# Kernel tuning notes

Measured on AMD Instinct MI355X. Metric: run time of the kernel, lower is better.

The kernel has to match this reference:

```python
import jax, jax.numpy as jnp
import numpy as np

B, T, H, V, N_AT, KC, MAX_NB = 512, 64, 512, 780, 40, 4, 8
NMSG = B * T + 1  # message table size; slot 0 = zero padding vector


def setup_inputs() -> dict:
    key = jax.random.key(0)
    ks = jax.random.split(key, 24)
    s = 0.02
    f32 = jnp.float32
    w = lambda k, shp: jax.random.normal(k, shp, f32) * s
    inp = {}
    inp["node_rep"] = jax.random.normal(ks[0], (B, N_AT, H), f32)
    inp["clique_idx"] = jax.random.randint(ks[1], (B, T, KC), 0, N_AT)
    inp["root_clique_idx"] = jax.random.randint(ks[2], (B, KC), 0, N_AT)
    inp["nei_h_idx"] = jax.random.randint(ks[3], (B, T, MAX_NB), 0, NMSG)
    inp["nei_o_idx"] = jax.random.randint(ks[4], (B, T, MAX_NB), 0, NMSG)
    inp["root_nei_idx"] = jax.random.randint(ks[5], (B, MAX_NB), 0, NMSG)
    inp["direction"] = jax.random.randint(ks[6], (B, T), 0, 2)
    inp["pred_target"] = jax.random.randint(ks[7], (B, T), 0, V)
    inp["W_z_w"] = w(ks[8], (2 * H, H)); inp["W_z_b"] = jnp.zeros((H,), f32)
    inp["W_r_w"] = w(ks[9], (H, H));     inp["W_r_b"] = jnp.zeros((H,), f32)
    inp["U_r_w"] = w(ks[10], (H, H))  # no bias in torch U_r
    inp["W_h_w"] = w(ks[11], (2 * H, H)); inp["W_h_b"] = jnp.zeros((H,), f32)
    inp["W_w"] = w(ks[12], (H, H));     inp["W_b"] = jnp.zeros((H,), f32)
    inp["U_w"] = w(ks[13], (2 * H, H)); inp["U_b"] = jnp.zeros((H,), f32)
    inp["W_o_w"] = w(ks[14], (H, V));   inp["W_o_b"] = jnp.zeros((V,), f32)
    inp["U_s_w"] = w(ks[15], (H, 1));   inp["U_s_b"] = jnp.zeros((1,), f32)
    return inp


def _gru(x, h_nei, W_z_w, W_z_b, W_r_w, W_r_b, U_r_w, W_h_w, W_h_b):
    # x: [B,H]; h_nei: [B,MAX_NB,H]  (tree-GRU from the torch GRU() helper)
    sum_h = h_nei.sum(axis=1)
    z = jax.nn.sigmoid(jnp.concatenate([x, sum_h], axis=1) @ W_z_w + W_z_b)
    r = jax.nn.sigmoid((x @ W_r_w + W_r_b)[:, None, :] + h_nei @ U_r_w)
    sum_g = (r * h_nei).sum(axis=1)
    pre_h = jnp.tanh(jnp.concatenate([x, sum_g], axis=1) @ W_h_w + W_h_b)
    return (1.0 - z) * sum_h + z * pre_h


def reference(node_rep, clique_idx, root_clique_idx, nei_h_idx, nei_o_idx,
              root_nei_idx, direction, pred_target,
              W_z_w, W_z_b, W_r_w, W_r_b, U_r_w, W_h_w, W_h_b,
              W_w, W_b, U_w, U_b, W_o_w, W_o_b, U_s_w, U_s_b):
    dt = node_rep.dtype
    b_ar = jnp.arange(B)
    # x features: sum of node_rep over clique atom indices (torch index_select+sum)
    x_all = node_rep[b_ar[:, None, None], clique_idx].sum(axis=2)      # [B,T,H]
    root_x = node_rep[b_ar[:, None], root_clique_idx].sum(axis=1)      # [B,H]
    msg_ids = b_ar[:, None] * T + jnp.arange(T)[None, :] + 1           # [B,T]
    table0 = jnp.zeros((NMSG, H), dt)                                  # h dict -> flat table

    def step(table, xs):
        x_t, h_idx, o_idx, mid = xs
        h_nei = table[h_idx]                      # [B,MAX_NB,H] gather (excl. parent, pre-padded)
        new_h = _gru(x_t, h_nei, W_z_w, W_z_b, W_r_w, W_r_b, U_r_w, W_h_w, W_h_b)
        o = table[o_idx].sum(axis=1)              # [B,H] all-neighbor sum for stop head
        table = table.at[mid].set(new_h)          # scatter message back (h[x,y] = new_h)
        return table, (new_h, o)

    xs = (x_all.transpose(1, 0, 2), nei_h_idx.transpose(1, 0, 2),
          nei_o_idx.transpose(1, 0, 2), msg_ids.T)
    table, (new_h_all, o_all) = jax.lax.scan(step, table0, xs)
    new_h_all = new_h_all.transpose(1, 0, 2).reshape(B * T, H)         # [BT,H]
    o_all = o_all.transpose(1, 0, 2)                                   # [B,T,H]

    # stop head: all steps + final root step (target 0)
    stop_h = jnp.concatenate([x_all, o_all], axis=2).reshape(B * T, 2 * H)
    root_o = table[root_nei_idx].sum(axis=1)
    root_stop = jnp.concatenate([root_x, root_o], axis=1)
    stop_hiddens = jnp.concatenate([stop_h, root_stop], axis=0)        # [BT+B,2H]
    stop_targets = jnp.concatenate([direction.reshape(-1).astype(dt), jnp.zeros((B,), dt)])
    stop_scores = (jax.nn.relu(stop_hiddens @ U_w + U_b) @ U_s_w + U_s_b)[:, 0]
    # BCEWithLogits, sum reduction, / len(mol_batch)
    stop_loss = jnp.sum(jax.nn.softplus(stop_scores) - stop_scores * stop_targets) / B
    stop_acc = jnp.mean(((stop_scores >= 0).astype(dt) == stop_targets).astype(dt))

    # pred head on new_h where direction == 1
    pred_scores = jax.nn.relu(new_h_all @ W_w + W_b) @ W_o_w + W_o_b   # [BT,V]
    logp = jax.nn.log_softmax(pred_scores, axis=-1)
    tgt = pred_target.reshape(-1)
    ce = -jnp.take_along_axis(logp, tgt[:, None], axis=1)[:, 0]
    pmask = (direction.reshape(-1) == 1).astype(dt)
    pred_loss = jnp.sum(ce * pmask) / B                                # CE sum / len(mol_batch)
    preds = jnp.argmax(pred_scores, axis=1)
    pred_acc = jnp.sum((preds == tgt).astype(dt) * pmask) / jnp.sum(pmask)
    return (pred_loss, stop_loss, pred_acc, stop_acc)
```

## Files before the change

### kernel.cpp

```cpp
#include <hip/hip_runtime.h>
#include <math.h>

constexpr int B    = 512;
constexpr int T    = 64;
constexpr int H    = 512;
constexpr int V    = 780;
constexpr int N_AT = 40;
constexpr int KC   = 4;
constexpr int NB   = 8;
constexpr int BT   = B * T;
constexpr int NMSG = BT + 1;

template<int ASRC, int NSEG, int EPI>
__device__ __forceinline__ void gemm_core(
    float* smem, int bx, int by,
    const float* __restrict__ A1, const float* __restrict__ A2, int lda,
    const float* __restrict__ W, const float* __restrict__ bias,
    float* __restrict__ C, int ldc,
    const int* __restrict__ gidx, int gt, const float* __restrict__ table,
    const float* __restrict__ node_rep, const int* __restrict__ cliq,
    const float* __restrict__ o_all,
    const int* __restrict__ rci, const int* __restrict__ rni,
    const float* __restrict__ Ez, const float* __restrict__ Esh,
    const float* __restrict__ Usw, float* __restrict__ partial)
{
    float* As = smem;
    float* Ws = smem + 32 * 68;
    const int tid  = threadIdx.x;
    const int row0 = bx * 64;
    const int col0 = by * 64;
    const int tm   = tid >> 4;
    const int tn   = tid & 15;

    float acc[4][4] = {};

    const int ar0 = tid >> 5;
    const int ac  = tid & 31;
    const int wk0 = tid >> 6;
    const int wc  = tid & 63;

    for (int seg = 0; seg < NSEG; ++seg) {
        const float* Aseg = seg ? A2 : A1;
        const float* Wseg = W + (size_t)seg * H * H;
        for (int k0 = 0; k0 < H; k0 += 32) {
#pragma unroll
            for (int it = 0; it < 8; ++it) {
                const int r    = ar0 + it * 8;
                const int grow = row0 + r;
                float v;
                if (ASRC == 0) {
                    v = Aseg[(size_t)grow * lda + k0 + ac];
                } else if (ASRC == 1) {
                    const int gi = gidx[((grow >> 3) * T + gt) * NB + (grow & 7)];
                    v = table[(size_t)gi * H + k0 + ac];
                } else if (ASRC == 2) {
                    const int* ci = cliq + (size_t)grow * KC;
                    const int  b  = grow >> 6;
                    v = 0.f;
#pragma unroll
                    for (int j = 0; j < KC; ++j)
                        v += node_rep[((size_t)b * N_AT + ci[j]) * H + k0 + ac];
                } else {
                    if (grow < BT) {
                        if (seg == 0) {
                            const int* ci = cliq + (size_t)grow * KC;
                            const int  b  = grow >> 6;
                            v = 0.f;
#pragma unroll
                            for (int j = 0; j < KC; ++j)
                                v += node_rep[((size_t)b * N_AT + ci[j]) * H + k0 + ac];
                        } else {
                            v = o_all[(size_t)grow * H + k0 + ac];
                        }
                    } else {
                        const int b = grow - BT;
                        v = 0.f;
                        if (seg == 0) {
#pragma unroll
                            for (int j = 0; j < KC; ++j)
                                v += node_rep[((size_t)b * N_AT + rci[b * KC + j]) * H + k0 + ac];
                        } else {
#pragma unroll
                            for (int n = 0; n < NB; ++n)
                                v += table[(size_t)rni[b * NB + n] * H + k0 + ac];
                        }
                    }
                }
                As[(size_t)ac * 68 + r] = v;
                const int kk = wk0 + it * 4;
                Ws[(size_t)kk * 68 + wc] = Wseg[(size_t)(k0 + kk) * H + col0 + wc];
            }
            __syncthreads();
#pragma unroll
            for (int kk = 0; kk < 32; ++kk) {
                float a[4], w[4];
                *(float4*)a = *(const float4*)&As[kk * 68 + tm * 4];
                *(float4*)w = *(const float4*)&Ws[kk * 68 + tn * 4];
#pragma unroll
                for (int i = 0; i < 4; ++i)
#pragma unroll
                    for (int j = 0; j < 4; ++j)
                        acc[i][j] = fmaf(a[i], w[j], acc[i][j]);
            }
            __syncthreads();
        }
    }

    if (EPI == 4) {
        float* sred = smem + 2 * 32 * 68;
#pragma unroll
        for (int i = 0; i < 4; ++i) {
            float s = 0.f;
#pragma unroll
            for (int j = 0; j < 4; ++j) {
                const int ccol = col0 + tn * 4 + j;
                float val = acc[i][j] + bias[ccol];
                val = fmaxf(val, 0.f);
                s += val * Usw[ccol];
            }
            sred[(size_t)(tm * 4 + i) * 17 + tn] = s;
        }
        __syncthreads();
        if (tid < 64) {
            float s = 0.f;
#pragma unroll
            for (int t2 = 0; t2 < 16; ++t2) s += sred[(size_t)tid * 17 + t2];
            partial[(size_t)(row0 + tid) * 8 + by] = s;
        }
    } else {
#pragma unroll
        for (int i = 0; i < 4; ++i) {
            const int r = row0 + tm * 4 + i;
            float out[4];
#pragma unroll
            for (int j = 0; j < 4; ++j) {
                const int ccol = col0 + tn * 4 + j;
                float val = acc[i][j] + (bias ? bias[ccol] : 0.f);
                if (EPI == 1) {
                    val = 1.f / (1.f + expf(-val));
                } else if (EPI == 2) {
                    const float ph = tanhf(val);
                    const float zz = Ez[(size_t)r * H + ccol];
                    const float sh = Esh[(size_t)r * H + ccol];
                    val = (1.f - zz) * sh + zz * ph;
                } else if (EPI == 3) {
                    val = fmaxf(val, 0.f);
                }
                out[j] = val;
            }
            *(float4*)&C[(size_t)r * ldc + col0 + tn * 4] = *(float4*)out;
        }
    }
}

constexpr size_t SM_GEMM = (size_t)(2 * 32 * 68) * 4;
constexpr size_t SM_STOP = (size_t)(2 * 32 * 68 + 64 * 17) * 4;

template<int ASRC, int NSEG, int EPI>
__global__ __launch_bounds__(256)
void gemm_g(const float* __restrict__ A1, const float* __restrict__ A2, int lda,
            const float* __restrict__ W, const float* __restrict__ bias,
            float* __restrict__ C, int ldc,
            const int* __restrict__ gidx, int gt, const float* __restrict__ table,
            const float* __restrict__ node_rep, const int* __restrict__ cliq,
            const float* __restrict__ o_all,
            const int* __restrict__ rci, const int* __restrict__ rni,
            const float* __restrict__ Ez, const float* __restrict__ Esh,
            const float* __restrict__ Usw, float* __restrict__ partial)
{
    extern __shared__ float smem[];
    gemm_core<ASRC, NSEG, EPI>(smem, blockIdx.x, blockIdx.y, A1, A2, lda, W, bias,
                               C, ldc, gidx, gt, table, node_rep, cliq, o_all,
                               rci, rni, Ez, Esh, Usw, partial);
}

__global__ __launch_bounds__(256)
void step1_kernel(const int* __restrict__ nei_h, int t, const float* __restrict__ table,
                  const float* __restrict__ Urw, float* __restrict__ hU,
                  const float* __restrict__ xs, const float* __restrict__ Wzw,
                  const float* __restrict__ Wzb, float* __restrict__ zb)
{
    extern __shared__ float smem[];
    if (blockIdx.x < 64) {
        gemm_core<1, 1, 0>(smem, blockIdx.x, blockIdx.y, nullptr, nullptr, 0,
                           Urw, nullptr, hU, H, nei_h, t, table,
                           nullptr, nullptr, nullptr, nullptr, nullptr,
                           nullptr, nullptr, nullptr, nullptr);
    } else {
        gemm_core<0, 2, 1>(smem, blockIdx.x - 64, blockIdx.y, xs, xs + H, 2 * H,
                           Wzw, Wzb, zb, H, nullptr, 0, nullptr,
                           nullptr, nullptr, nullptr, nullptr, nullptr,
                           nullptr, nullptr, nullptr, nullptr);
    }
}

__global__ __launch_bounds__(256)
void pre2_kernel(const float* __restrict__ node_rep, const int* __restrict__ clique_idx,
                 const int* __restrict__ nei_h, const int* __restrict__ nei_o,
                 const float* __restrict__ table,
                 float* __restrict__ xs, float* __restrict__ hs, float* __restrict__ ss,
                 float* __restrict__ sumh, float* __restrict__ oDst, int oStride, int t)
{
    const int i = blockIdx.x * 256 + threadIdx.x;
    const int b = i >> 9, h = i & 511;
    const int* ci = clique_idx + ((size_t)b * T + t) * KC;
    float x = 0.f;
#pragma unroll
    for (int k = 0; k < KC; ++k)
        x += node_rep[((size_t)b * N_AT + ci[k]) * H + h];
    const int* hi = nei_h + ((size_t)b * T + t) * NB;
    const int* oi = nei_o + ((size_t)b * T + t) * NB;
    float sh = 0.f, so = 0.f;
#pragma unroll
    for (int n = 0; n < NB; ++n) {
        sh += table[(size_t)hi[n] * H + h];
        so += table[(size_t)oi[n] * H + h];
    }
    xs[(size_t)b * 1024 + h]       = x;
    xs[(size_t)b * 1024 + 512 + h] = sh;
    hs[(size_t)b * 1024 + h]       = x;
    ss[(size_t)b * 1024 + h]       = x;
    sumh[i] = sh;
    oDst[(size_t)b * oStride + h] = so;
}

__global__ __launch_bounds__(256)
void rsum2_kernel(const float* __restrict__ xrP, int xrStride,
                  const float* __restrict__ hU, const float* __restrict__ table,
                  const int* __restrict__ nei_h, float* __restrict__ hs, int t)
{
    const int i = blockIdx.x * 256 + threadIdx.x;
    const int b = i >> 9, h = i & 511;
    const int* hi = nei_h + ((size_t)b * T + t) * NB;
    const float xrv = xrP[(size_t)b * xrStride + h];
    float s = 0.f;
#pragma unroll
    for (int n = 0; n < NB; ++n) {
        const float hu = hU[((size_t)b * NB + n) * H + h];
        const float r  = 1.f / (1.f + expf(-(xrv + hu)));
        s += r * table[(size_t)hi[n] * H + h];
    }
    hs[(size_t)b * 1024 + 512 + h] = s;
}

__global__ __launch_bounds__(256)
void rootpre_kernel(const float* __restrict__ node_rep, const int* __restrict__ rci,
                    const int* __restrict__ rni, const float* __restrict__ table,
                    float* __restrict__ ss)
{
    const int i = blockIdx.x * 256 + threadIdx.x;
    const int b = i >> 9, h = i & 511;
    float x = 0.f;
#pragma unroll
    for (int k = 0; k < KC; ++k)
        x += node_rep[((size_t)b * N_AT + rci[b * KC + k]) * H + h];
    float so = 0.f;
#pragma unroll
    for (int n = 0; n < NB; ++n)
        so += table[(size_t)rni[b * NB + n] * H + h];
    ss[(size_t)b * 1024 + h]       = x;
    ss[(size_t)b * 1024 + 512 + h] = so;
}

__global__ __launch_bounds__(64)
void stopdot_kernel(const float* __restrict__ s1, const float* __restrict__ Usw,
                    const float* __restrict__ Usb,
                    float* __restrict__ out, int outStride, int outBase)
{
    const int b = blockIdx.x;
    const int lane = threadIdx.x;
    const float* row = s1 + (size_t)b * H;
    float s = 0.f;
    for (int h = lane; h < H; h += 64) s += row[h] * Usw[h];
#pragma unroll
    for (int off = 32; off; off >>= 1) s += __shfl_down(s, off);
    if (lane == 0) out[outBase + b * outStride] = s + Usb[0];
}

__global__ __launch_bounds__(256)
void stoploss_kernel(const float* __restrict__ scores, const int* __restrict__ direction,
                     float* __restrict__ accum)
{
    const int i = blockIdx.x * 256 + threadIdx.x;
    float loss = 0.f, acc = 0.f;
    if (i < BT + B) {
        const float s   = scores[i];
        const float tgt = (i < BT) ? (float)direction[i] : 0.f;
        loss = fmaxf(s, 0.f) - s * tgt + log1pf(expf(-fabsf(s)));
        const float p = (s >= 0.f) ? 1.f : 0.f;
        acc = (p == tgt) ? 1.f : 0.f;
    }
#pragma unroll
    for (int off = 32; off; off >>= 1) {
        loss += __shfl_down(loss, off);
        acc  += __shfl_down(acc, off);
    }
    if ((threadIdx.x & 63) == 0) {
        atomicAdd(&accum[3], loss);
        atomicAdd(&accum[4], acc);
    }
}

__global__ __launch_bounds__(256)
void stopfin_kernel(const float* __restrict__ partial, const float* __restrict__ Usb,
                    const int* __restrict__ direction, float* __restrict__ accum)
{
    const int i = blockIdx.x * 256 + threadIdx.x;
    float loss = 0.f, acc = 0.f;
    {
        float s = Usb[0];
#pragma unroll
        for (int cb = 0; cb < 8; ++cb) s += partial[(size_t)i * 8 + cb];
        const float tgt = (i < BT) ? (float)direction[i] : 0.f;
        loss = fmaxf(s, 0.f) - s * tgt + log1pf(expf(-fabsf(s)));
        const float p = (s >= 0.f) ? 1.f : 0.f;
        acc = (p == tgt) ? 1.f : 0.f;
    }
#pragma unroll
    for (int off = 32; off; off >>= 1) {
        loss += __shfl_down(loss, off);
        acc  += __shfl_down(acc, off);
    }
    if ((threadIdx.x & 63) == 0) {
        atomicAdd(&accum[3], loss);
        atomicAdd(&accum[4], acc);
    }
}

__global__ __launch_bounds__(256)
void ce_kernel(const float* __restrict__ s1_all, const float* __restrict__ Wo,
               const float* __restrict__ Wob, const int* __restrict__ direction,
               const int* __restrict__ ptgt, float* __restrict__ accum)
{
    __shared__ float s1T[512 * 34];
    __shared__ float Ws[32 * 68];
    __shared__ float blk[3];
    const int tid  = threadIdx.x;
    const int row0 = blockIdx.x * 32;

    for (int idx = tid; idx < 32 * 512; idx += 256) {
        const int r = idx >> 9, k = idx & 511;
        s1T[(size_t)k * 34 + r] = s1_all[(size_t)(row0 + r) * H + k];
    }
    if (tid < 3) blk[tid] = 0.f;
    __syncthreads();

    const int tm = tid >> 4, tn = tid & 15;
    const int tgt0 = ptgt[row0 + tm * 2];
    const int tgt1 = ptgt[row0 + tm * 2 + 1];
    float m0 = -1e30f, m1 = -1e30f, ss0 = 0.f, ss1 = 0.f, st0 = 0.f, st1 = 0.f;
    float bv0 = -1e30f, bv1 = -1e30f;
    int   bj0 = 0, bj1 = 0;

    for (int ct = 0; ct < 13; ++ct) {
        const int col0 = ct * 64;
        float acc[2][4] = {};
        for (int k0 = 0; k0 < 512; k0 += 32) {
#pragma unroll
            for (int it = 0; it < 8; ++it) {
                const int idx = tid + it * 256;
                const int kk = idx >> 6, cc = idx & 63;
                const int col = col0 + cc;
                Ws[(size_t)kk * 68 + cc] = (col < V) ? Wo[(size_t)(k0 + kk) * V + col] : 0.f;
            }
            __syncthreads();
#pragma unroll
            for (int kk = 0; kk < 32; ++kk) {
                const float a0 = s1T[(size_t)(k0 + kk) * 34 + tm * 2];
                const float a1 = s1T[(size_t)(k0 + kk) * 34 + tm * 2 + 1];
                float w[4];
                *(float4*)w = *(const float4*)&Ws[kk * 68 + tn * 4];
#pragma unroll
                for (int j = 0; j < 4; ++j) {
                    acc[0][j] = fmaf(a0, w[j], acc[0][j]);
                    acc[1][j] = fmaf(a1, w[j], acc[1][j]);
                }
            }
            __syncthreads();
        }
#pragma unroll
        for (int j = 0; j < 4; ++j) {
            const int col = col0 + tn * 4 + j;
            if (col < V) {
                const float wb  = Wob[col];
                const float sc0 = acc[0][j] + wb;
                const float sc1 = acc[1][j] + wb;
                if (sc0 > m0) { ss0 = ss0 * expf(m0 - sc0) + 1.f; m0 = sc0; }
                else          { ss0 += expf(sc0 - m0); }
                if (sc1 > m1) { ss1 = ss1 * expf(m1 - sc1) + 1.f; m1 = sc1; }
                else          { ss1 += expf(sc1 - m1); }
                if (sc0 > bv0) { bv0 = sc0; bj0 = col; }
                if (sc1 > bv1) { bv1 = sc1; bj1 = col; }
                if (col == tgt0) st0 = sc0;
                if (col == tgt1) st1 = sc1;
            }
        }
    }

#pragma unroll
    for (int off = 1; off < 16; off <<= 1) {
        float om, os;
        om = __shfl_xor(m0, off); os = __shfl_xor(ss0, off);
        { const float nm = fmaxf(m0, om); ss0 = ss0 * expf(m0 - nm) + os * expf(om - nm); m0 = nm; }
        om = __shfl_xor(m1, off); os = __shfl_xor(ss1, off);
        { const float nm = fmaxf(m1, om); ss1 = ss1 * expf(m1 - nm) + os * expf(om - nm); m1 = nm; }
        float obv; int obj;
        obv = __shfl_xor(bv0, off); obj = __shfl_xor(bj0, off);
        if (obv > bv0 || (obv == bv0 && obj < bj0)) { bv0 = obv; bj0 = obj; }
        obv = __shfl_xor(bv1, off); obj = __shfl_xor(bj1, off);
        if (obv > bv1 || (obv == bv1 && obj < bj1)) { bv1 = obv; bj1 = obj; }
        st0 += __shfl_xor(st0, off);
        st1 += __shfl_xor(st1, off);
    }
    if (tn == 0) {
        float ce_s = 0.f, cnt = 0.f, corr = 0.f;
        {
            const int row = row0 + tm * 2;
            if (direction[row] == 1) {
                ce_s += (m0 + logf(ss0)) - st0; cnt += 1.f;
                corr += (bj0 == tgt0) ? 1.f : 0.f;
            }
        }
        {
            const int row = row0 + tm * 2 + 1;
            if (direction[row] == 1) {
                ce_s += (m1 + logf(ss1)) - st1; cnt += 1.f;
                corr += (bj1 == tgt1) ? 1.f : 0.f;
            }
        }
        atomicAdd(&blk[0], ce_s); atomicAdd(&blk[1], cnt); atomicAdd(&blk[2], corr);
    }
    __syncthreads();
    if (tid == 0) {
        atomicAdd(&accum[0], blk[0]);
        atomicAdd(&accum[1], blk[1]);
        atomicAdd(&accum[2], blk[2]);
    }
}

constexpr int PH_ROWS = 8;
__global__ __launch_bounds__(256)
void predhead_kernel(const float* __restrict__ table,
                     const float* __restrict__ Ww, const float* __restrict__ Wb,
                     const float* __restrict__ Wo, const float* __restrict__ Wob,
                     const int* __restrict__ direction, const int* __restrict__ ptgt,
                     float* __restrict__ accum)
{
    __shared__ float hs[PH_ROWS][520];
    __shared__ float s1s[PH_ROWS][520];
    const int row0 = blockIdx.x * PH_ROWS;
    const int tid  = threadIdx.x;
    for (int i = tid; i < PH_ROWS * H; i += 256) {
        const int r = i >> 9, c = i & 511;
        hs[r][c] = table[(size_t)(row0 + r + 1) * H + c];
    }
    __syncthreads();
    const int r  = tid >> 5;
    const int tx = tid & 31;
    for (int j = 0; j < 16; ++j) {
        const int c = tx + j * 32;
        float acc = Wb[c];
        for (int k = 0; k < H; ++k) acc += hs[r][k] * Ww[(size_t)k * H + c];
        s1s[r][c] = fmaxf(acc, 0.f);
    }
    __syncthreads();
    const int row = row0 + r;
    const int tgt = ptgt[row];
    float m = -1e30f, ssum = 0.f, stgt = 0.f;
    float bestv = -1e30f; int bestj = 0;
    for (int v = tx; v < V; v += 32) {
        float sc = Wob[v];
        const float* wcol = Wo + v;
        for (int k = 0; k < H; ++k) sc += s1s[r][k] * wcol[(size_t)k * V];
        if (sc > m) { ssum = ssum * expf(m - sc) + 1.f; m = sc; }
        else        { ssum += expf(sc - m); }
        if (sc > bestv) { bestv = sc; bestj = v; }
        if (v == tgt) stgt = sc;
    }
#pragma unroll
    for (int off = 1; off < 32; off <<= 1) {
        const float om = __shfl_xor(m, off);
        const float os = __shfl_xor(ssum, off);
        const float nm = fmaxf(m, om);
        ssum = ssum * expf(m - nm) + os * expf(om - nm);
        m = nm;
        const float obv = __shfl_xor(bestv, off);
        const int   obj = __shfl_xor(bestj, off);
        if (obv > bestv || (obv == bestv && obj < bestj)) { bestv = obv; bestj = obj; }
        stgt += __shfl_xor(stgt, off);
    }
    if (tx == 0) {
        const float ce   = (m + logf(ssum)) - stgt;
        const float mask = (direction[row] == 1) ? 1.f : 0.f;
        const float corr = (bestj == tgt) ? 1.f : 0.f;
        atomicAdd(&accum[0], ce * mask);
        atomicAdd(&accum[1], mask);
        atomicAdd(&accum[2], corr * mask);
    }
}

__global__ void finalize_kernel(const float* __restrict__ accum, float* __restrict__ out)
{
    if (threadIdx.x == 0) {
        out[0] = accum[0] / (float)B;
        out[1] = accum[3] / (float)B;
        out[2] = accum[2] / accum[1];
        out[3] = accum[4] / (float)(BT + B);
    }
}

extern "C" void kernel_launch(void* const* d_in, const int* in_sizes, int n_in,
                              void* d_out, int out_size, void* d_ws, size_t ws_size,
                              hipStream_t stream)
{
    (void)in_sizes; (void)n_in; (void)out_size;

    const float* node_rep        = (const float*)d_in[0];
    const int*   clique_idx      = (const int*)d_in[1];
    const int*   root_clique_idx = (const int*)d_in[2];
    const int*   nei_h_idx       = (const int*)d_in[3];
    const int*   nei_o_idx       = (const int*)d_in[4];
    const int*   root_nei_idx    = (const int*)d_in[5];
    const int*   direction       = (const int*)d_in[6];
    const int*   pred_target     = (const int*)d_in[7];
    const float* W_z_w = (const float*)d_in[8];
    const float* W_z_b = (const float*)d_in[9];
    const float* W_r_w = (const float*)d_in[10];
    const float* W_r_b = (const float*)d_in[11];
    const float* U_r_w = (const float*)d_in[12];
    const float* W_h_w = (const float*)d_in[13];
    const float* W_h_b = (const float*)d_in[14];
    const float* W_w   = (const float*)d_in[15];
    const float* W_b   = (const float*)d_in[16];
    const float* U_w   = (const float*)d_in[17];
    const float* U_b   = (const float*)d_in[18];
    const float* W_o_w = (const float*)d_in[19];
    const float* W_o_b = (const float*)d_in[20];
    const float* U_s_w = (const float*)d_in[21];
    const float* U_s_b = (const float*)d_in[22];

    float* ws = (float*)d_ws;
    size_t off = 0;
    auto alloc = [&](size_t n) { float* p = ws + off; off += n; return p; };

    float* table  = alloc((size_t)NMSG * H);
    float* hU     = alloc((size_t)B * NB * H);
    float* xs     = alloc((size_t)B * 2 * H);
    float* hs     = alloc((size_t)B * 2 * H);
    float* ss     = alloc((size_t)B * 2 * H);
    float* sumh   = alloc((size_t)B * H);
    float* zb     = alloc((size_t)B * H);
    float* xr     = alloc((size_t)B * H);
    float* stop_scores = alloc(BT + B);
    float* accum  = alloc(8);

    const size_t availF = ws_size / sizeof(float);
    float *s1_all = nullptr, *o_all = nullptr, *partial = nullptr, *xr_all = nullptr;
    if (off + (size_t)BT * H <= availF)                 s1_all = alloc((size_t)BT * H);
    if (off + (size_t)BT * H + (size_t)(BT + B) * 8 <= availF) {
        o_all   = alloc((size_t)BT * H);
        partial = alloc((size_t)(BT + B) * 8);
    }
    if (off + (size_t)BT * H <= availF)                 xr_all = alloc((size_t)BT * H);

    hipMemsetAsync(table, 0, (size_t)NMSG * H * sizeof(float), stream);
    hipMemsetAsync(accum, 0, 8 * sizeof(float), stream);

    const int  BH_blocks = (B * H) / 256;
    const dim3 gSmall(8, 8);
    const dim3 gStep(72, 8);

    if (xr_all) {
        gemm_g<2, 1, 0><<<dim3(BT / 64, 8), 256, SM_GEMM, stream>>>(
            nullptr, nullptr, 0, W_r_w, W_r_b, xr_all, H,
            nullptr, 0, nullptr, node_rep, clique_idx,
            nullptr, nullptr, nullptr, nullptr, nullptr, nullptr, nullptr);
    }

    for (int t = 0; t < T; ++t) {
        float* oDst    = o_all ? (o_all + (size_t)t * H) : (ss + H);
        const int oStr = o_all ? (T * H) : (2 * H);
        pre2_kernel<<<BH_blocks, 256, 0, stream>>>(node_rep, clique_idx, nei_h_idx,
                                                   nei_o_idx, table, xs, hs, ss,
                                                   sumh, oDst, oStr, t);
        step1_kernel<<<gStep, 256, SM_GEMM, stream>>>(nei_h_idx, t, table, U_r_w, hU,
                                                      xs, W_z_w, W_z_b, zb);
        if (!xr_all) {
            gemm_g<0, 1, 0><<<gSmall, 256, SM_GEMM, stream>>>(
                xs, nullptr, 2 * H, W_r_w, W_r_b, xr, H,
                nullptr, 0, nullptr, nullptr, nullptr,
                nullptr, nullptr, nullptr, nullptr, nullptr, nullptr, nullptr);
        }
        const float* xrP   = xr_all ? (xr_all + (size_t)t * H) : xr;
        const int    xrStr = xr_all ? (T * H) : H;
        rsum2_kernel<<<BH_blocks, 256, 0, stream>>>(xrP, xrStr, hU, table,
                                                    nei_h_idx, hs, t);
        gemm_g<0, 2, 2><<<gSmall, 256, SM_GEMM, stream>>>(
            hs, hs + H, 2 * H, W_h_w, W_h_b, table + (size_t)(t + 1) * H, T * H,
            nullptr, 0, nullptr, nullptr, nullptr,
            nullptr, nullptr, nullptr, zb, sumh, nullptr, nullptr);
        if (!o_all) {
            gemm_g<0, 2, 3><<<gSmall, 256, SM_GEMM, stream>>>(
                ss, ss + H, 2 * H, U_w, U_b, zb, H,
                nullptr, 0, nullptr, nullptr, nullptr,
                nullptr, nullptr, nullptr, nullptr, nullptr, nullptr, nullptr);
            stopdot_kernel<<<B, 64, 0, stream>>>(zb, U_s_w, U_s_b, stop_scores, T, t);
        }
    }

    if (o_all) {
        gemm_g<3, 2, 4><<<dim3((BT + B) / 64, 8), 256, SM_STOP, stream>>>(
            nullptr, nullptr, 0, U_w, U_b, nullptr, 0,
            nullptr, 0, table, node_rep, clique_idx,
            o_all, root_clique_idx, root_nei_idx, nullptr, nullptr, U_s_w, partial);
        stopfin_kernel<<<(BT + B) / 256, 256, 0, stream>>>(partial, U_s_b, direction, accum);
    } else {
        rootpre_kernel<<<BH_blocks, 256, 0, stream>>>(node_rep, root_clique_idx,
                                                      root_nei_idx, table, ss);
        gemm_g<0, 2, 3><<<gSmall, 256, SM_GEMM, stream>>>(
            ss, ss + H, 2 * H, U_w, U_b, zb, H,
            nullptr, 0, nullptr, nullptr, nullptr,
            nullptr, nullptr, nullptr, nullptr, nullptr, nullptr, nullptr);
        stopdot_kernel<<<B, 64, 0, stream>>>(zb, U_s_w, U_s_b, stop_scores, 1, BT);
        stoploss_kernel<<<(BT + B + 255) / 256, 256, 0, stream>>>(stop_scores, direction, accum);
    }

    if (s1_all) {
        gemm_g<0, 1, 3><<<dim3(BT / 64, 8), 256, SM_GEMM, stream>>>(
            table + H, nullptr, H, W_w, W_b, s1_all, H,
            nullptr, 0, nullptr, nullptr, nullptr,
            nullptr, nullptr, nullptr, nullptr, nullptr, nullptr, nullptr);
        ce_kernel<<<BT / 32, 256, 0, stream>>>(s1_all, W_o_w, W_o_b,
                                               direction, pred_target, accum);
    } else {
        predhead_kernel<<<BT / PH_ROWS, 256, 0, stream>>>(table, W_w, W_b, W_o_w, W_o_b,
                                                          direction, pred_target, accum);
    }

    finalize_kernel<<<1, 64, 0, stream>>>(accum, (float*)d_out);
}
```

Baseline: 13.48 ms.

## Fuse per-step gather and reset-gate kernels into GEMM A-tile loaders

Removes the separate pre2 and rsum2 elementwise kernels from each time step. Their gathers (clique sums, neighbour message sums, sigmoid-gated reset sums) now run inside the GEMM A-tile loading of a combined stepA kernel and of the W_h GEMM. The W_r GEMM and the nei_o gather become extra block ranges of stepA. This halves launches per step and drops the xs/hs staging buffers. The cost is that gather and expf work is recomputed by every column block of each GEMM, and the h-GEMM runs on only 64 blocks. Neighbour rows belonging to the current step are explicitly zeroed, because those rows are written concurrently by the same kernel.

```diff
diff --git a/kernel.cpp b/kernel.cpp
--- a/kernel.cpp
+++ b/kernel.cpp
@@ -22,7 +22,9 @@
     const float* __restrict__ o_all,
     const int* __restrict__ rci, const int* __restrict__ rni,
     const float* __restrict__ Ez, const float* __restrict__ Esh,
-    const float* __restrict__ Usw, float* __restrict__ partial)
+    const float* __restrict__ Usw, float* __restrict__ partial,
+    const float* __restrict__ xrP, int xrStride,
+    const float* __restrict__ hUin, float* __restrict__ sumhOut)
 {
     float* As = smem;
     float* Ws = smem + 32 * 68;
@@ -60,7 +62,7 @@
 #pragma unroll
                     for (int j = 0; j < KC; ++j)
                         v += node_rep[((size_t)b * N_AT + ci[j]) * H + k0 + ac];
-                } else {
+                } else if (ASRC == 3) {
                     if (grow < BT) {
                         if (seg == 0) {
                             const int* ci = cliq + (size_t)grow * KC;
@@ -83,6 +85,45 @@
 #pragma unroll
                             for (int n = 0; n < NB; ++n)
                                 v += table[(size_t)rni[b * NB + n] * H + k0 + ac];
+                        }
+                    }
+                } else if (ASRC == 5) {
+                    const int b = grow;
+                    if (seg == 0) {
+                        const int* ci = cliq + ((size_t)b * T + gt) * KC;
+                        v = 0.f;
+#pragma unroll
+                        for (int j = 0; j < KC; ++j)
+                            v += node_rep[((size_t)b * N_AT + ci[j]) * H + k0 + ac];
+                    } else {
+                        const int* hi = gidx + ((size_t)b * T + gt) * NB;
+                        v = 0.f;
+#pragma unroll
+                        for (int n = 0; n < NB; ++n)
+                            v += table[(size_t)hi[n] * H + k0 + ac];
+                        if (sumhOut && by == 0)
+                            sumhOut[(size_t)b * H + k0 + ac] = v;
+                    }
+                } else {
+                    const int b = grow;
+                    if (seg == 0) {
+                        const int* ci = cliq + ((size_t)b * T + gt) * KC;
+                        v = 0.f;
+#pragma unroll
+                        for (int j = 0; j < KC; ++j)
+                            v += node_rep[((size_t)b * N_AT + ci[j]) * H + k0 + ac];
+                    } else {
+                        const int* hi = gidx + ((size_t)b * T + gt) * NB;
+                        const float xrv = xrP[(size_t)b * xrStride + k0 + ac];
+                        v = 0.f;
+#pragma unroll
+                        for (int n = 0; n < NB; ++n) {
+                            const int idx = hi[n];
+                            const float hu = hUin[((size_t)b * NB + n) * H + k0 + ac];
+                            const float rr = 1.f / (1.f + expf(-(xrv + hu)));
+                            float hv = table[(size_t)idx * H + k0 + ac];
+                            if (idx != 0 && ((idx - 1) & 63) == gt) hv = 0.f;
+                            v += rr * hv;
                         }
                     }
                 }
@@ -166,81 +207,61 @@
             const float* __restrict__ o_all,
             const int* __restrict__ rci, const int* __restrict__ rni,
             const float* __restrict__ Ez, const float* __restrict__ Esh,
-            const float* __restrict__ Usw, float* __restrict__ partial)
+            const float* __restrict__ Usw, float* __restrict__ partial,
+            const float* __restrict__ xrP, int xrStride,
+            const float* __restrict__ hUin, float* __restrict__ sumhOut)
 {
     extern __shared__ float smem[];
     gemm_core<ASRC, NSEG, EPI>(smem, blockIdx.x, blockIdx.y, A1, A2, lda, W, bias,
                                C, ldc, gidx, gt, table, node_rep, cliq, o_all,
-                               rci, rni, Ez, Esh, Usw, partial);
+                               rci, rni, Ez, Esh, Usw, partial,
+                               xrP, xrStride, hUin, sumhOut);
 }
 
 __global__ __launch_bounds__(256)
-void step1_kernel(const int* __restrict__ nei_h, int t, const float* __restrict__ table,
+void stepA_kernel(const int* __restrict__ nei_h, const int* __restrict__ nei_o, int t,
+                  const float* __restrict__ table, const float* __restrict__ node_rep,
+                  const int* __restrict__ cliq,
                   const float* __restrict__ Urw, float* __restrict__ hU,
-                  const float* __restrict__ xs, const float* __restrict__ Wzw,
-                  const float* __restrict__ Wzb, float* __restrict__ zb)
+                  const float* __restrict__ Wzw, const float* __restrict__ Wzb,
+                  float* __restrict__ zb, float* __restrict__ sumh,
+                  float* __restrict__ xtDst, float* __restrict__ oDst, int xoStride,
+                  const float* __restrict__ Wrw, const float* __restrict__ Wrb,
+                  float* __restrict__ xrOut)
 {
     extern __shared__ float smem[];
-    if (blockIdx.x < 64) {
-        gemm_core<1, 1, 0>(smem, blockIdx.x, blockIdx.y, nullptr, nullptr, 0,
-                           Urw, nullptr, hU, H, nei_h, t, table,
-                           nullptr, nullptr, nullptr, nullptr, nullptr,
-                           nullptr, nullptr, nullptr, nullptr);
+    const int bx = blockIdx.x, by = blockIdx.y;
+    if (bx < 64) {
+        gemm_core<1, 1, 0>(smem, bx, by, nullptr, nullptr, 0, Urw, nullptr, hU, H,
+                           nei_h, t, table, nullptr, nullptr, nullptr, nullptr, nullptr,
+                           nullptr, nullptr, nullptr, nullptr, nullptr, 0, nullptr, nullptr);
+    } else if (bx < 72) {
+        gemm_core<5, 2, 1>(smem, bx - 64, by, nullptr, nullptr, 0, Wzw, Wzb, zb, H,
+                           nei_h, t, table, node_rep, cliq, nullptr, nullptr, nullptr,
+                           nullptr, nullptr, nullptr, nullptr, nullptr, 0, nullptr, sumh);
+    } else if (bx < 200) {
+        const int og = (bx - 72) * 8 + by;
+        const int i  = og * 256 + threadIdx.x;
+        const int b  = i >> 9, h = i & 511;
+        const int* oi = nei_o + ((size_t)b * T + t) * NB;
+        float so = 0.f;
+#pragma unroll
+        for (int n = 0; n < NB; ++n)
+            so += table[(size_t)oi[n] * H + h];
+        oDst[(size_t)b * xoStride + h] = so;
+        if (xtDst) {
+            const int* ci = cliq + ((size_t)b * T + t) * KC;
+            float x = 0.f;
+#pragma unroll
+            for (int j = 0; j < KC; ++j)
+                x += node_rep[((size_t)b * N_AT + ci[j]) * H + h];
+            xtDst[(size_t)b * xoStride + h] = x;
+        }
     } else {
-        gemm_core<0, 2, 1>(smem, blockIdx.x - 64, blockIdx.y, xs, xs + H, 2 * H,
-                           Wzw, Wzb, zb, H, nullptr, 0, nullptr,
-                           nullptr, nullptr, nullptr, nullptr, nullptr,
-                           nullptr, nullptr, nullptr, nullptr);
-    }
-}
-
-__global__ __launch_bounds__(256)
-void pre2_kernel(const float* __restrict__ node_rep, const int* __restrict__ clique_idx,
-                 const int* __restrict__ nei_h, const int* __restrict__ nei_o,
-                 const float* __restrict__ table,
-                 float* __restrict__ xs, float* __restrict__ hs, float* __restrict__ ss,
-                 float* __restrict__ sumh, float* __restrict__ oDst, int oStride, int t)
-{
-    const int i = blockIdx.x * 256 + threadIdx.x;
-    const int b = i >> 9, h = i & 511;
-    const int* ci = clique_idx + ((size_t)b * T + t) * KC;
-    float x = 0.f;
-#pragma unroll
-    for (int k = 0; k < KC; ++k)
-        x += node_rep[((size_t)b * N_AT + ci[k]) * H + h];
-    const int* hi = nei_h + ((size_t)b * T + t) * NB;
-    const int* oi = nei_o + ((size_t)b * T + t) * NB;
-    float sh = 0.f, so = 0.f;
-#pragma unroll
-    for (int n = 0; n < NB; ++n) {
-        sh += table[(size_t)hi[n] * H + h];
-        so += table[(size_t)oi[n] * H + h];
-    }
-    xs[(size_t)b * 1024 + h]       = x;
-    xs[(size_t)b * 1024 + 512 + h] = sh;
-    hs[(size_t)b * 1024 + h]       = x;
-    ss[(size_t)b * 1024 + h]       = x;
-    sumh[i] = sh;
-    oDst[(size_t)b * oStride + h] = so;
-}
-
-__global__ __launch_bounds__(256)
-void rsum2_kernel(const float* __restrict__ xrP, int xrStride,
-                  const float* __restrict__ hU, const float* __restrict__ table,
-                  const int* __restrict__ nei_h, float* __restrict__ hs, int t)
-{
-    const int i = blockIdx.x * 256 + threadIdx.x;
-    const int b = i >> 9, h = i & 511;
-    const int* hi = nei_h + ((size_t)b * T + t) * NB;
-    const float xrv = xrP[(size_t)b * xrStride + h];
-    float s = 0.f;
-#pragma unroll
-    for (int n = 0; n < NB; ++n) {
-        const float hu = hU[((size_t)b * NB + n) * H + h];
-        const float r  = 1.f / (1.f + expf(-(xrv + hu)));
-        s += r * table[(size_t)hi[n] * H + h];
-    }
-    hs[(size_t)b * 1024 + 512 + h] = s;
+        gemm_core<5, 1, 0>(smem, bx - 200, by, nullptr, nullptr, 0, Wrw, Wrb, xrOut, H,
+                           nei_h, t, table, node_rep, cliq, nullptr, nullptr, nullptr,
+                           nullptr, nullptr, nullptr, nullptr, nullptr, 0, nullptr, nullptr);
+    }
 }
 
 __global__ __launch_bounds__(256)
@@ -545,8 +566,6 @@
 
     float* table  = alloc((size_t)NMSG * H);
     float* hU     = alloc((size_t)B * NB * H);
-    float* xs     = alloc((size_t)B * 2 * H);
-    float* hs     = alloc((size_t)B * 2 * H);
     float* ss     = alloc((size_t)B * 2 * H);
     float* sumh   = alloc((size_t)B * H);
     float* zb     = alloc((size_t)B * H);
@@ -566,44 +585,43 @@
     hipMemsetAsync(table, 0, (size_t)NMSG * H * sizeof(float), stream);
     hipMemsetAsync(accum, 0, 8 * sizeof(float), stream);
 
-    const int  BH_blocks = (B * H) / 256;
     const dim3 gSmall(8, 8);
-    const dim3 gStep(72, 8);
 
     if (xr_all) {
         gemm_g<2, 1, 0><<<dim3(BT / 64, 8), 256, SM_GEMM, stream>>>(
             nullptr, nullptr, 0, W_r_w, W_r_b, xr_all, H,
             nullptr, 0, nullptr, node_rep, clique_idx,
-            nullptr, nullptr, nullptr, nullptr, nullptr, nullptr, nullptr);
-    }
+            nullptr, nullptr, nullptr, nullptr, nullptr, nullptr, nullptr,
+            nullptr, 0, nullptr, nullptr);
+    }
+
+    const dim3 gStepA(xr_all ? 200 : 208, 8);
 
     for (int t = 0; t < T; ++t) {
         float* oDst    = o_all ? (o_all + (size_t)t * H) : (ss + H);
+        float* xtDst   = o_all ? nullptr : ss;
         const int oStr = o_all ? (T * H) : (2 * H);
-        pre2_kernel<<<BH_blocks, 256, 0, stream>>>(node_rep, clique_idx, nei_h_idx,
-                                                   nei_o_idx, table, xs, hs, ss,
-                                                   sumh, oDst, oStr, t);
-        step1_kernel<<<gStep, 256, SM_GEMM, stream>>>(nei_h_idx, t, table, U_r_w, hU,
-                                                      xs, W_z_w, W_z_b, zb);
-        if (!xr_all) {
-            gemm_g<0, 1, 0><<<gSmall, 256, SM_GEMM, stream>>>(
-                xs, nullptr, 2 * H, W_r_w, W_r_b, xr, H,
-                nullptr, 0, nullptr, nullptr, nullptr,
-                nullptr, nullptr, nullptr, nullptr, nullptr, nullptr, nullptr);
-        }
+
+        stepA_kernel<<<gStepA, 256, SM_GEMM, stream>>>(
+            nei_h_idx, nei_o_idx, t, table, node_rep, clique_idx,
+            U_r_w, hU, W_z_w, W_z_b, zb, sumh, xtDst, oDst, oStr,
+            W_r_w, W_r_b, xr);
+
         const float* xrP   = xr_all ? (xr_all + (size_t)t * H) : xr;
         const int    xrStr = xr_all ? (T * H) : H;
-        rsum2_kernel<<<BH_blocks, 256, 0, stream>>>(xrP, xrStr, hU, table,
-                                                    nei_h_idx, hs, t);
-        gemm_g<0, 2, 2><<<gSmall, 256, SM_GEMM, stream>>>(
-            hs, hs + H, 2 * H, W_h_w, W_h_b, table + (size_t)(t + 1) * H, T * H,
-            nullptr, 0, nullptr, nullptr, nullptr,
-            nullptr, nullptr, nullptr, zb, sumh, nullptr, nullptr);
+
+        gemm_g<6, 2, 2><<<gSmall, 256, SM_GEMM, stream>>>(
+            nullptr, nullptr, 0, W_h_w, W_h_b, table + (size_t)(t + 1) * H, T * H,
+            nei_h_idx, t, table, node_rep, clique_idx,
+            nullptr, nullptr, nullptr, zb, sumh, nullptr, nullptr,
+            xrP, xrStr, hU, nullptr);
+
         if (!o_all) {
             gemm_g<0, 2, 3><<<gSmall, 256, SM_GEMM, stream>>>(
                 ss, ss + H, 2 * H, U_w, U_b, zb, H,
                 nullptr, 0, nullptr, nullptr, nullptr,
-                nullptr, nullptr, nullptr, nullptr, nullptr, nullptr, nullptr);
+                nullptr, nullptr, nullptr, nullptr, nullptr, nullptr, nullptr,
+                nullptr, 0, nullptr, nullptr);
             stopdot_kernel<<<B, 64, 0, stream>>>(zb, U_s_w, U_s_b, stop_scores, T, t);
         }
     }
@@ -612,15 +630,17 @@
         gemm_g<3, 2, 4><<<dim3((BT + B) / 64, 8), 256, SM_STOP, stream>>>(
             nullptr, nullptr, 0, U_w, U_b, nullptr, 0,
             nullptr, 0, table, node_rep, clique_idx,
-            o_all, root_clique_idx, root_nei_idx, nullptr, nullptr, U_s_w, partial);
+            o_all, root_clique_idx, root_nei_idx, nullptr, nullptr, U_s_w, partial,
+            nullptr, 0, nullptr, nullptr);
         stopfin_kernel<<<(BT + B) / 256, 256, 0, stream>>>(partial, U_s_b, direction, accum);
     } else {
-        rootpre_kernel<<<BH_blocks, 256, 0, stream>>>(node_rep, root_clique_idx,
-                                                      root_nei_idx, table, ss);
+        rootpre_kernel<<<(B * H) / 256, 256, 0, stream>>>(node_rep, root_clique_idx,
+                                                          root_nei_idx, table, ss);
         gemm_g<0, 2, 3><<<gSmall, 256, SM_GEMM, stream>>>(
             ss, ss + H, 2 * H, U_w, U_b, zb, H,
             nullptr, 0, nullptr, nullptr, nullptr,
-            nullptr, nullptr, nullptr, nullptr, nullptr, nullptr, nullptr);
+            nullptr, nullptr, nullptr, nullptr, nullptr, nullptr, nullptr,
+            nullptr, 0, nullptr, nullptr);
         stopdot_kernel<<<B, 64, 0, stream>>>(zb, U_s_w, U_s_b, stop_scores, 1, BT);
         stoploss_kernel<<<(BT + B + 255) / 256, 256, 0, stream>>>(stop_scores, direction, accum);
     }
@@ -629,7 +649,8 @@
         gemm_g<0, 1, 3><<<dim3(BT / 64, 8), 256, SM_GEMM, stream>>>(
             table + H, nullptr, H, W_w, W_b, s1_all, H,
             nullptr, 0, nullptr, nullptr, nullptr,
-            nullptr, nullptr, nullptr, nullptr, nullptr, nullptr, nullptr);
+            nullptr, nullptr, nullptr, nullptr, nullptr, nullptr, nullptr,
+            nullptr, 0, nullptr, nullptr);
         ce_kernel<<<BT / 32, 256, 0, stream>>>(s1_all, W_o_w, W_o_b,
                                                direction, pred_target, accum);
     } else {
```

After: 39.03 ms. 2.89x slower.
